# Kernel tuning notes

Measured on AMD Instinct MI355X. Metric: run time of the kernel, lower is better.

## Reference

```python
import jax, jax.numpy as jnp
import numpy as np

N = 4000      # number_of_sensors
D_IN = 128    # input feature dim
D_OUT = 128   # output feature dim
E_DIM = 16    # node embedding dim
B = 8         # batch size


def setup_inputs() -> dict:
    key = jax.random.key(0)
    k_x, k_e1, k_e2, k_w = jax.random.split(key, 4)
    x = jax.random.normal(k_x, (B, N, D_IN), dtype=jnp.float32)
    E1 = jax.random.normal(k_e1, (N, E_DIM), dtype=jnp.float32)
    E2 = jax.random.normal(k_e2, (N, E_DIM), dtype=jnp.float32)
    W = jax.random.normal(k_w, (D_IN, D_OUT), dtype=jnp.float32) * (1.0 / np.sqrt(D_IN))
    b = jnp.zeros((D_OUT,), dtype=jnp.float32)
    return {"x": x, "E1": E1, "E2": E2, "W": W, "b": b}


def reference(x, E1, E2, W, b):
    # Adaptive adjacency from node embeddings: A = softmax(relu(E1 @ E2^T), axis=-1)
    logits = jax.nn.relu(jnp.einsum('nd,md->nm', E1, E2))  # [N, N]
    adj = jax.nn.softmax(logits, axis=-1)                  # row-normalized adjacency
    # Graph aggregation then feature transform: relu(A @ X @ W + b)
    agg = jnp.einsum('nm,bmf->bnf', adj, x)                # [B, N, D_IN]
    out = jax.nn.relu(jnp.einsum('bnf,fo->bno', agg, W) + b)  # [B, N, D_OUT]
    return out
```

## Files before the change

kernel.cpp:

```cpp
#include <hip/hip_runtime.h>
#include <hip/hip_bf16.h>

#define NSEN 4000
#define NP   4096
#define DIN  128
#define DOUT 128
#define EDIM 16
#define BATCH 8

typedef __attribute__((ext_vector_type(8))) short bf16x8;
typedef __attribute__((ext_vector_type(4))) float f32x4;

__device__ __forceinline__ unsigned short f2bf(float f) {
  unsigned int u = __float_as_uint(f);
  unsigned int r = (u + 0x7FFFu + ((u >> 16) & 1u)) >> 16;
  return (unsigned short)r;
}
__device__ __forceinline__ float bf2f(unsigned short s) {
  unsigned int u = ((unsigned int)s) << 16;
  return __uint_as_float(u);
}

__device__ __forceinline__ void gl_lds16(const void* g, void* l) {
  __builtin_amdgcn_global_load_lds((const __attribute__((address_space(1))) void*)g,
                                   (__attribute__((address_space(3))) void*)l, 16, 0, 0);
}

__global__ __launch_bounds__(512) void k_prep(const float* __restrict__ E1,
                                              const float* __restrict__ E2,
                                              const float* __restrict__ W,
                                              const float* __restrict__ x,
                                              unsigned short* __restrict__ adjp,
                                              float* __restrict__ rinv,
                                              unsigned short* __restrict__ yt) {
  __shared__ float rsum[8][16];
  __shared__ unsigned short wlds[128 * 136];
  const int bx = blockIdx.x;
  const int tid = threadIdx.x;
  const int lane = tid & 63, wv = tid >> 6;
  const int lr = lane & 15, lq = lane >> 4;

  if (bx >= 250) {
    {
      const int fr = tid >> 5;
      const int o4 = tid & 31;
#pragma unroll
      for (int r8 = 0; r8 < 8; r8++) {
        const int f = fr + r8 * 16;
        float4 w4 = *(const float4*)&W[(size_t)f * DOUT + o4 * 4];
        wlds[(o4 * 4 + 0) * 136 + f] = f2bf(w4.x);
        wlds[(o4 * 4 + 1) * 136 + f] = f2bf(w4.y);
        wlds[(o4 * 4 + 2) * 136 + f] = f2bf(w4.z);
        wlds[(o4 * 4 + 3) * 136 + f] = f2bf(w4.w);
      }
    }
    __syncthreads();

    const int yi = bx - 250;
    const int b  = yi >> 4;
    const int m0 = (yi & 15) * 256;
    const int mh = wv >> 2;
    const int os = wv & 3;

    bf16x8 af[2][4];
#pragma unroll
    for (int ot = 0; ot < 2; ot++) {
      const int ob = os * 32 + ot * 16 + lr;
#pragma unroll
      for (int ks = 0; ks < 4; ks++)
        af[ot][ks] = *(const bf16x8*)&wlds[ob * 136 + ks * 32 + lq * 8];
    }

#pragma unroll
    for (int cc = 0; cc < 4; cc++) {
#pragma unroll
      for (int mtile = 0; mtile < 2; mtile++) {
        const int mb = m0 + cc * 64 + mh * 32 + mtile * 16;
        const int m = mb + lr;
        bf16x8 bx8[4];
        if (m < NSEN) {
          const float* xp = &x[((size_t)b * NSEN + m) * DIN + lq * 8];
#pragma unroll
          for (int ks = 0; ks < 4; ks++) {
            float4 v0 = *(const float4*)(xp + ks * 32);
            float4 v1 = *(const float4*)(xp + ks * 32 + 4);
            bx8[ks][0] = (short)f2bf(v0.x); bx8[ks][1] = (short)f2bf(v0.y);
            bx8[ks][2] = (short)f2bf(v0.z); bx8[ks][3] = (short)f2bf(v0.w);
            bx8[ks][4] = (short)f2bf(v1.x); bx8[ks][5] = (short)f2bf(v1.y);
            bx8[ks][6] = (short)f2bf(v1.z); bx8[ks][7] = (short)f2bf(v1.w);
          }
        } else {
#pragma unroll
          for (int ks = 0; ks < 4; ks++)
#pragma unroll
            for (int j = 0; j < 8; j++) bx8[ks][j] = 0;
        }
#pragma unroll
        for (int ot = 0; ot < 2; ot++) {
          f32x4 c = (f32x4){0.f, 0.f, 0.f, 0.f};
#pragma unroll
          for (int ks = 0; ks < 4; ks++)
            c = __builtin_amdgcn_mfma_f32_16x16x32_bf16(af[ot][ks], bx8[ks], c, 0, 0, 0);
#pragma unroll
          for (int i = 0; i < 4; i++)
            yt[(size_t)(b * 128 + os * 32 + ot * 16 + lq * 4 + i) * NP + mb + lr] = f2bf(c[i]);
        }
      }
    }
    return;
  }

  const int n0 = bx * 16;

  float a[8];
  {
    const float* e1p = &E1[(size_t)(n0 + lr) * EDIM + (lq & 1) * 8];
    *(float4*)&a[0] = *(const float4*)e1p;
    *(float4*)&a[4] = *(const float4*)(e1p + 4);
  }
  bf16x8 af1, af2;
#pragma unroll
  for (int j = 0; j < 8; j++) {
    unsigned short hs = f2bf(a[j]);
    af1[j] = (short)hs;
    float lo = a[j] - bf2f(hs);
    af2[j] = (lq < 2) ? (short)f2bf(lo) : (short)0;
  }

  float rs[4] = {0.f, 0.f, 0.f, 0.f};
  for (int t = wv; t < NSEN / 16; t += 8) {
    const int m = t * 16 + lr;
    float bv[8];
    const float* e2p = &E2[(size_t)m * EDIM + (lq & 1) * 8];
    *(float4*)&bv[0] = *(const float4*)e2p;
    *(float4*)&bv[4] = *(const float4*)(e2p + 4);
    bf16x8 bfrag;
#pragma unroll
    for (int j = 0; j < 8; j++) {
      unsigned short hs = f2bf(bv[j]);
      if (lq < 2) bfrag[j] = (short)hs;
      else        bfrag[j] = (short)f2bf(bv[j] - bf2f(hs));
    }
    f32x4 c = (f32x4){0.f, 0.f, 0.f, 0.f};
    c = __builtin_amdgcn_mfma_f32_16x16x32_bf16(af1, bfrag, c, 0, 0, 0);
    c = __builtin_amdgcn_mfma_f32_16x16x32_bf16(af2, bfrag, c, 0, 0, 0);
#pragma unroll
    for (int i = 0; i < 4; i++) {
      float p = __expf(fmaxf(c[i], 0.f));
      rs[i] += p;
      adjp[(size_t)(n0 + lq * 4 + i) * NP + t * 16 + lr] = f2bf(p);
    }
  }
  for (int i = tid; i < 16 * (NP - NSEN); i += 512) {
    int r = i / (NP - NSEN), c = i % (NP - NSEN);
    adjp[(size_t)(n0 + r) * NP + NSEN + c] = 0;
  }
#pragma unroll
  for (int i = 0; i < 4; i++) {
    rs[i] += __shfl_xor(rs[i], 1, 64);
    rs[i] += __shfl_xor(rs[i], 2, 64);
    rs[i] += __shfl_xor(rs[i], 4, 64);
    rs[i] += __shfl_xor(rs[i], 8, 64);
  }
  if (lr == 0) {
#pragma unroll
    for (int i = 0; i < 4; i++) rsum[wv][lq * 4 + i] = rs[i];
  }
  __syncthreads();
  if (tid < 16) {
    float s = 0.f;
#pragma unroll
    for (int w = 0; w < 8; w++) s += rsum[w][tid];
    rinv[n0 + tid] = 1.0f / s;
  }
}

__global__ __launch_bounds__(256, 2) void k_gemm1(const unsigned short* __restrict__ A,
                                                  const unsigned short* __restrict__ Bt,
                                                  unsigned short* __restrict__ part) {
  __shared__ __align__(16) unsigned short smem[32768];
  const int tid = threadIdx.x;
  const int lane = tid & 63, wv = tid >> 6;
  const int wr = wv >> 1, wc = wv & 1;
  const int lr = lane & 15, lq = lane >> 4;
  const int gx = blockIdx.x;
  const int m0 = (gx >> 1) * 128;
  const int kb0 = (gx & 1) * 2048;
  const int b  = blockIdx.y;
  const int c0 = b * 128;
  unsigned short* tA0 = smem;
  unsigned short* tB0 = smem + 16384;

  f32x4 acc[4][4];
#pragma unroll
  for (int p = 0; p < 4; p++)
#pragma unroll
    for (int q = 0; q < 4; q++) acc[p][q] = (f32x4){0.f, 0.f, 0.f, 0.f};

#define STAGE(bufi, kb)                                                              \
  {                                                                                  \
    _Pragma("unroll")                                                                \
    for (int s = 0; s < 4; s++) {                                                    \
      int idx = s * 256 + tid;                                                       \
      int row = idx >> 3;                                                            \
      int kc = ((idx & 7) ^ (row & 7)) << 3;                                         \
      gl_lds16(&A[(size_t)(m0 + row) * NP + (kb) + kc], &tA0[(bufi)*8192 + idx*8]);  \
      gl_lds16(&Bt[(size_t)(c0 + row) * NP + (kb) + kc], &tB0[(bufi)*8192 + idx*8]); \
    }                                                                                \
  }

  STAGE(0, kb0);

  for (int it = 0; it < 32; ++it) {
    const int cur = it & 1;
    if (it < 31) {
      STAGE(cur ^ 1, kb0 + (it + 1) * 64);
      asm volatile("s_waitcnt vmcnt(8)" ::: "memory");
    } else {
      asm volatile("s_waitcnt vmcnt(0)" ::: "memory");
    }
    __builtin_amdgcn_s_barrier();

    bf16x8 af0[4], bf0[4], af1[4], bf1[4];
    {
      const int koff0 = (lq * 8) ^ ((lr & 7) << 3);
#pragma unroll
      for (int p = 0; p < 4; p++)
        af0[p] = *(const bf16x8*)&tA0[cur * 8192 + (wr * 64 + p * 16 + lr) * 64 + koff0];
#pragma unroll
      for (int q = 0; q < 4; q++)
        bf0[q] = *(const bf16x8*)&tB0[cur * 8192 + (wc * 64 + q * 16 + lr) * 64 + koff0];
    }
    __builtin_amdgcn_sched_barrier(0);
    {
      const int koff1 = (32 + lq * 8) ^ ((lr & 7) << 3);
#pragma unroll
      for (int p = 0; p < 4; p++)
        af1[p] = *(const bf16x8*)&tA0[cur * 8192 + (wr * 64 + p * 16 + lr) * 64 + koff1];
#pragma unroll
      for (int q = 0; q < 4; q++)
        bf1[q] = *(const bf16x8*)&tB0[cur * 8192 + (wc * 64 + q * 16 + lr) * 64 + koff1];
    }
    asm volatile("s_waitcnt lgkmcnt(8)" ::: "memory");
    __builtin_amdgcn_sched_barrier(0);
    __builtin_amdgcn_s_setprio(1);
#pragma unroll
    for (int p = 0; p < 4; p++)
#pragma unroll
      for (int q = 0; q < 4; q++)
        acc[p][q] = __builtin_amdgcn_mfma_f32_16x16x32_bf16(af0[p], bf0[q], acc[p][q], 0, 0, 0);
    asm volatile("s_waitcnt lgkmcnt(0)" ::: "memory");
    __builtin_amdgcn_sched_barrier(0);
#pragma unroll
    for (int p = 0; p < 4; p++)
#pragma unroll
      for (int q = 0; q < 4; q++)
        acc[p][q] = __builtin_amdgcn_mfma_f32_16x16x32_bf16(af1[p], bf1[q], acc[p][q], 0, 0, 0);
    __builtin_amdgcn_s_setprio(0);
    __builtin_amdgcn_s_barrier();
  }
#undef STAGE

  const int kh = gx & 1;
  unsigned short* pdst = part + ((size_t)(kh * BATCH + b) * NP + m0) * DIN;
#pragma unroll
  for (int p = 0; p < 4; p++)
#pragma unroll
    for (int q = 0; q < 4; q++) {
      const int col = wc * 64 + q * 16 + lr;
#pragma unroll
      for (int i = 0; i < 4; i++) {
        const int row = wr * 64 + p * 16 + lq * 4 + i;
        pdst[row * DIN + col] = f2bf(acc[p][q][i]);
      }
    }
}

__global__ __launch_bounds__(256) void k_fin(const unsigned short* __restrict__ part,
                                             const float* __restrict__ rinv,
                                             const float* __restrict__ bias,
                                             float* __restrict__ out) {
  const int tid = threadIdx.x;
  const int nl = tid >> 4;
  const int ch = tid & 15;
  const int n  = blockIdx.x * 16 + nl;
  const int b  = blockIdx.y;
  const size_t base = ((size_t)b * NP + n) * DIN + ch * 8;
  const size_t khoff = (size_t)BATCH * NP * DIN;

  bf16x8 p0 = *(const bf16x8*)&part[base];
  bf16x8 p1 = *(const bf16x8*)&part[khoff + base];
  const float rv = rinv[n];
  float4 bb0 = *(const float4*)&bias[ch * 8];
  float4 bb1 = *(const float4*)&bias[ch * 8 + 4];
  float r[8];
#pragma unroll
  for (int j = 0; j < 8; j++) {
    float bbj = (j < 4) ? ((const float*)&bb0)[j] : ((const float*)&bb1)[j - 4];
    r[j] = fmaxf((bf2f((unsigned short)p0[j]) + bf2f((unsigned short)p1[j])) * rv + bbj, 0.f);
  }
  float* op = &out[((size_t)b * NSEN + n) * DOUT + ch * 8];
  *(float4*)op       = make_float4(r[0], r[1], r[2], r[3]);
  *(float4*)(op + 4) = make_float4(r[4], r[5], r[6], r[7]);
}

extern "C" void kernel_launch(void* const* d_in, const int* in_sizes, int n_in,
                              void* d_out, int out_size, void* d_ws, size_t ws_size,
                              hipStream_t stream) {
  const float* x    = (const float*)d_in[0];
  const float* E1   = (const float*)d_in[1];
  const float* E2   = (const float*)d_in[2];
  const float* W    = (const float*)d_in[3];
  const float* bias = (const float*)d_in[4];
  float* out = (float*)d_out;

  char* ws = (char*)d_ws;
  unsigned short* adjp = (unsigned short*)(ws);
  unsigned short* yt   = (unsigned short*)(ws + 33554432);
  float*          rinv = (float*)(ws + 33554432 + 8388608);
  unsigned short* part = (unsigned short*)(ws + 33554432 + 8388608 + 16384);

  k_prep<<<dim3(378), dim3(512), 0, stream>>>(E1, E2, W, x, adjp, rinv, yt);
  k_gemm1<<<dim3(64, BATCH), dim3(256), 0, stream>>>(adjp, yt, part);
  k_fin<<<dim3(250, BATCH), dim3(256), 0, stream>>>(part, rinv, bias, out);
}
```

Baseline: 77.46 us.

## Stage adjacency and Y writes through LDS, widen GEMM tiles, adaptive split-K

The prep kernel now stages the exp'd adjacency rows and the XW product in LDS before writing them back as coalesced 16-byte chunks, instead of scattering 2-byte stores. The Y-projection blocks are halved in size so more blocks share the work. The main GEMM becomes one 512-thread kernel with 256x256 tiles over a 4096x1024 output that covers all batches at once, and it picks 4-way or 2-way split-K depending on workspace size. The finalize kernel sums a variable number of K-slices. The costs are larger LDS and register use per block, and extra partial-sum traffic when 4-way split-K is chosen.

```diff
diff --git a/kernel.cpp b/kernel.cpp
--- a/kernel.cpp
+++ b/kernel.cpp
@@ -34,13 +34,15 @@
                                               float* __restrict__ rinv,
                                               unsigned short* __restrict__ yt) {
   __shared__ float rsum[8][16];
-  __shared__ unsigned short wlds[128 * 136];
+  __shared__ __align__(16) unsigned short pool[34816];
   const int bx = blockIdx.x;
   const int tid = threadIdx.x;
   const int lane = tid & 63, wv = tid >> 6;
   const int lr = lane & 15, lq = lane >> 4;
 
   if (bx >= 250) {
+    unsigned short* wlds = pool;
+    unsigned short* ylds = pool + 17408;
     {
       const int fr = tid >> 5;
       const int o4 = tid & 31;
@@ -57,8 +59,8 @@
     __syncthreads();
 
     const int yi = bx - 250;
-    const int b  = yi >> 4;
-    const int m0 = (yi & 15) * 256;
+    const int b  = yi >> 5;
+    const int m0 = (yi & 31) * 128;
     const int mh = wv >> 2;
     const int os = wv & 3;
 
@@ -72,44 +74,51 @@
     }
 
 #pragma unroll
-    for (int cc = 0; cc < 4; cc++) {
-#pragma unroll
-      for (int mtile = 0; mtile < 2; mtile++) {
-        const int mb = m0 + cc * 64 + mh * 32 + mtile * 16;
-        const int m = mb + lr;
-        bf16x8 bx8[4];
-        if (m < NSEN) {
-          const float* xp = &x[((size_t)b * NSEN + m) * DIN + lq * 8];
-#pragma unroll
-          for (int ks = 0; ks < 4; ks++) {
-            float4 v0 = *(const float4*)(xp + ks * 32);
-            float4 v1 = *(const float4*)(xp + ks * 32 + 4);
-            bx8[ks][0] = (short)f2bf(v0.x); bx8[ks][1] = (short)f2bf(v0.y);
-            bx8[ks][2] = (short)f2bf(v0.z); bx8[ks][3] = (short)f2bf(v0.w);
-            bx8[ks][4] = (short)f2bf(v1.x); bx8[ks][5] = (short)f2bf(v1.y);
-            bx8[ks][6] = (short)f2bf(v1.z); bx8[ks][7] = (short)f2bf(v1.w);
-          }
-        } else {
-#pragma unroll
-          for (int ks = 0; ks < 4; ks++)
-#pragma unroll
-            for (int j = 0; j < 8; j++) bx8[ks][j] = 0;
+    for (int mt = 0; mt < 4; mt++) {
+      const int mloc = mh * 64 + mt * 16;
+      const int m = m0 + mloc + lr;
+      bf16x8 bx8[4];
+      if (m < NSEN) {
+        const float* xp = &x[((size_t)b * NSEN + m) * DIN + lq * 8];
+#pragma unroll
+        for (int ks = 0; ks < 4; ks++) {
+          float4 v0 = *(const float4*)(xp + ks * 32);
+          float4 v1 = *(const float4*)(xp + ks * 32 + 4);
+          bx8[ks][0] = (short)f2bf(v0.x); bx8[ks][1] = (short)f2bf(v0.y);
+          bx8[ks][2] = (short)f2bf(v0.z); bx8[ks][3] = (short)f2bf(v0.w);
+          bx8[ks][4] = (short)f2bf(v1.x); bx8[ks][5] = (short)f2bf(v1.y);
+          bx8[ks][6] = (short)f2bf(v1.z); bx8[ks][7] = (short)f2bf(v1.w);
         }
-#pragma unroll
-        for (int ot = 0; ot < 2; ot++) {
-          f32x4 c = (f32x4){0.f, 0.f, 0.f, 0.f};
-#pragma unroll
-          for (int ks = 0; ks < 4; ks++)
-            c = __builtin_amdgcn_mfma_f32_16x16x32_bf16(af[ot][ks], bx8[ks], c, 0, 0, 0);
-#pragma unroll
-          for (int i = 0; i < 4; i++)
-            yt[(size_t)(b * 128 + os * 32 + ot * 16 + lq * 4 + i) * NP + mb + lr] = f2bf(c[i]);
-        }
-      }
+      } else {
+#pragma unroll
+        for (int ks = 0; ks < 4; ks++)
+#pragma unroll
+          for (int j = 0; j < 8; j++) bx8[ks][j] = 0;
+      }
+#pragma unroll
+      for (int ot = 0; ot < 2; ot++) {
+        f32x4 c = (f32x4){0.f, 0.f, 0.f, 0.f};
+#pragma unroll
+        for (int ks = 0; ks < 4; ks++)
+          c = __builtin_amdgcn_mfma_f32_16x16x32_bf16(af[ot][ks], bx8[ks], c, 0, 0, 0);
+#pragma unroll
+        for (int i = 0; i < 4; i++)
+          ylds[(os * 32 + ot * 16 + lq * 4 + i) * 136 + mloc + lr] = f2bf(c[i]);
+      }
+    }
+    __syncthreads();
+#pragma unroll
+    for (int s2 = 0; s2 < 4; s2++) {
+      int c = s2 * 512 + tid;
+      int row = c >> 4;
+      int mc = c & 15;
+      *(bf16x8*)&yt[(size_t)(b * 128 + row) * NP + m0 + mc * 8] =
+          *(const bf16x8*)&ylds[row * 136 + mc * 8];
     }
     return;
   }
 
+  unsigned short* bounce = pool;
   const int n0 = bx * 16;
 
   float a[8];
@@ -128,32 +137,46 @@
   }
 
   float rs[4] = {0.f, 0.f, 0.f, 0.f};
-  for (int t = wv; t < NSEN / 16; t += 8) {
-    const int m = t * 16 + lr;
-    float bv[8];
-    const float* e2p = &E2[(size_t)m * EDIM + (lq & 1) * 8];
-    *(float4*)&bv[0] = *(const float4*)e2p;
-    *(float4*)&bv[4] = *(const float4*)(e2p + 4);
-    bf16x8 bfrag;
-#pragma unroll
-    for (int j = 0; j < 8; j++) {
-      unsigned short hs = f2bf(bv[j]);
-      if (lq < 2) bfrag[j] = (short)hs;
-      else        bfrag[j] = (short)f2bf(bv[j] - bf2f(hs));
-    }
-    f32x4 c = (f32x4){0.f, 0.f, 0.f, 0.f};
-    c = __builtin_amdgcn_mfma_f32_16x16x32_bf16(af1, bfrag, c, 0, 0, 0);
-    c = __builtin_amdgcn_mfma_f32_16x16x32_bf16(af2, bfrag, c, 0, 0, 0);
-#pragma unroll
-    for (int i = 0; i < 4; i++) {
-      float p = __expf(fmaxf(c[i], 0.f));
-      rs[i] += p;
-      adjp[(size_t)(n0 + lq * 4 + i) * NP + t * 16 + lr] = f2bf(p);
-    }
-  }
-  for (int i = tid; i < 16 * (NP - NSEN); i += 512) {
-    int r = i / (NP - NSEN), c = i % (NP - NSEN);
-    adjp[(size_t)(n0 + r) * NP + NSEN + c] = 0;
+  for (int w0 = 0; w0 < 256; w0 += 64) {
+    if (w0 == 192) {
+      for (int z = tid; z < 16 * 96; z += 512) {
+        int zr = z / 96, zc = z % 96;
+        bounce[zr * 1040 + 58 * 16 + zc] = 0;
+      }
+    }
+    const int tend = (w0 + 64 < 250) ? (w0 + 64) : 250;
+    for (int t = w0 + wv; t < tend; t += 8) {
+      const int m = t * 16 + lr;
+      float bv[8];
+      const float* e2p = &E2[(size_t)m * EDIM + (lq & 1) * 8];
+      *(float4*)&bv[0] = *(const float4*)e2p;
+      *(float4*)&bv[4] = *(const float4*)(e2p + 4);
+      bf16x8 bfrag;
+#pragma unroll
+      for (int j = 0; j < 8; j++) {
+        unsigned short hs = f2bf(bv[j]);
+        if (lq < 2) bfrag[j] = (short)hs;
+        else        bfrag[j] = (short)f2bf(bv[j] - bf2f(hs));
+      }
+      f32x4 c = (f32x4){0.f, 0.f, 0.f, 0.f};
+      c = __builtin_amdgcn_mfma_f32_16x16x32_bf16(af1, bfrag, c, 0, 0, 0);
+      c = __builtin_amdgcn_mfma_f32_16x16x32_bf16(af2, bfrag, c, 0, 0, 0);
+#pragma unroll
+      for (int i = 0; i < 4; i++) {
+        float p = __expf(fmaxf(c[i], 0.f));
+        rs[i] += p;
+        bounce[(lq * 4 + i) * 1040 + (t - w0) * 16 + lr] = f2bf(p);
+      }
+    }
+    __syncthreads();
+#pragma unroll
+    for (int s2 = 0; s2 < 4; s2++) {
+      int cch = s2 * 512 + tid;
+      int row = cch >> 7, mc = cch & 127;
+      *(bf16x8*)&adjp[(size_t)(n0 + row) * NP + w0 * 16 + mc * 8] =
+          *(const bf16x8*)&bounce[row * 1040 + mc * 8];
+    }
+    __syncthreads();
   }
 #pragma unroll
   for (int i = 0; i < 4; i++) {
@@ -175,45 +198,45 @@
   }
 }
 
-__global__ __launch_bounds__(256, 2) void k_gemm1(const unsigned short* __restrict__ A,
-                                                  const unsigned short* __restrict__ Bt,
-                                                  unsigned short* __restrict__ part) {
-  __shared__ __align__(16) unsigned short smem[32768];
+__global__ __launch_bounds__(512, 2) void k_gemm(const unsigned short* __restrict__ A,
+                                                 const unsigned short* __restrict__ Bt,
+                                                 unsigned short* __restrict__ part,
+                                                 int nsteps) {
+  __shared__ __align__(16) unsigned short smem[65536];
+  unsigned short* tA0 = smem;
+  unsigned short* tB0 = smem + 32768;
   const int tid = threadIdx.x;
   const int lane = tid & 63, wv = tid >> 6;
-  const int wr = wv >> 1, wc = wv & 1;
+  const int wr = wv >> 2, wcn = wv & 3;
   const int lr = lane & 15, lq = lane >> 4;
-  const int gx = blockIdx.x;
-  const int m0 = (gx >> 1) * 128;
-  const int kb0 = (gx & 1) * 2048;
-  const int b  = blockIdx.y;
-  const int c0 = b * 128;
-  unsigned short* tA0 = smem;
-  unsigned short* tB0 = smem + 16384;
-
-  f32x4 acc[4][4];
-#pragma unroll
-  for (int p = 0; p < 4; p++)
+  const int kh = blockIdx.x >> 4;
+  const int m0 = (blockIdx.x & 15) * 256;
+  const int n0c = blockIdx.y * 256;
+  const int kb0 = kh * nsteps * 64;
+
+  f32x4 acc[8][4];
+#pragma unroll
+  for (int p = 0; p < 8; p++)
 #pragma unroll
     for (int q = 0; q < 4; q++) acc[p][q] = (f32x4){0.f, 0.f, 0.f, 0.f};
 
-#define STAGE(bufi, kb)                                                              \
-  {                                                                                  \
-    _Pragma("unroll")                                                                \
-    for (int s = 0; s < 4; s++) {                                                    \
-      int idx = s * 256 + tid;                                                       \
-      int row = idx >> 3;                                                            \
-      int kc = ((idx & 7) ^ (row & 7)) << 3;                                         \
-      gl_lds16(&A[(size_t)(m0 + row) * NP + (kb) + kc], &tA0[(bufi)*8192 + idx*8]);  \
-      gl_lds16(&Bt[(size_t)(c0 + row) * NP + (kb) + kc], &tB0[(bufi)*8192 + idx*8]); \
-    }                                                                                \
+#define STAGE(bufi, kb)                                                                 \
+  {                                                                                     \
+    _Pragma("unroll")                                                                   \
+    for (int s = 0; s < 4; s++) {                                                       \
+      int idx = s * 512 + tid;                                                          \
+      int row = idx >> 3;                                                               \
+      int kc = ((idx & 7) ^ (row & 7)) << 3;                                            \
+      gl_lds16(&A[(size_t)(m0 + row) * NP + (kb) + kc], &tA0[(bufi)*16384 + idx*8]);    \
+      gl_lds16(&Bt[(size_t)(n0c + row) * NP + (kb) + kc], &tB0[(bufi)*16384 + idx*8]);  \
+    }                                                                                   \
   }
 
   STAGE(0, kb0);
 
-  for (int it = 0; it < 32; ++it) {
+  for (int it = 0; it < nsteps; ++it) {
     const int cur = it & 1;
-    if (it < 31) {
+    if (it < nsteps - 1) {
       STAGE(cur ^ 1, kb0 + (it + 1) * 64);
       asm volatile("s_waitcnt vmcnt(8)" ::: "memory");
     } else {
@@ -221,57 +244,58 @@
     }
     __builtin_amdgcn_s_barrier();
 
-    bf16x8 af0[4], bf0[4], af1[4], bf1[4];
     {
-      const int koff0 = (lq * 8) ^ ((lr & 7) << 3);
-#pragma unroll
-      for (int p = 0; p < 4; p++)
-        af0[p] = *(const bf16x8*)&tA0[cur * 8192 + (wr * 64 + p * 16 + lr) * 64 + koff0];
+      const int koff = (lq * 8) ^ ((lr & 7) << 3);
+      bf16x8 af[8], bf[4];
+#pragma unroll
+      for (int p = 0; p < 8; p++)
+        af[p] = *(const bf16x8*)&tA0[cur * 16384 + (wr * 128 + p * 16 + lr) * 64 + koff];
 #pragma unroll
       for (int q = 0; q < 4; q++)
-        bf0[q] = *(const bf16x8*)&tB0[cur * 8192 + (wc * 64 + q * 16 + lr) * 64 + koff0];
-    }
-    __builtin_amdgcn_sched_barrier(0);
+        bf[q] = *(const bf16x8*)&tB0[cur * 16384 + (wcn * 64 + q * 16 + lr) * 64 + koff];
+      asm volatile("s_waitcnt lgkmcnt(0)" ::: "memory");
+      __builtin_amdgcn_sched_barrier(0);
+      __builtin_amdgcn_s_setprio(1);
+#pragma unroll
+      for (int p = 0; p < 8; p++)
+#pragma unroll
+        for (int q = 0; q < 4; q++)
+          acc[p][q] = __builtin_amdgcn_mfma_f32_16x16x32_bf16(af[p], bf[q], acc[p][q], 0, 0, 0);
+      __builtin_amdgcn_s_setprio(0);
+    }
     {
-      const int koff1 = (32 + lq * 8) ^ ((lr & 7) << 3);
-#pragma unroll
-      for (int p = 0; p < 4; p++)
-        af1[p] = *(const bf16x8*)&tA0[cur * 8192 + (wr * 64 + p * 16 + lr) * 64 + koff1];
+      const int koff = (32 + lq * 8) ^ ((lr & 7) << 3);
+      bf16x8 af[8], bf[4];
+#pragma unroll
+      for (int p = 0; p < 8; p++)
+        af[p] = *(const bf16x8*)&tA0[cur * 16384 + (wr * 128 + p * 16 + lr) * 64 + koff];
 #pragma unroll
       for (int q = 0; q < 4; q++)
-        bf1[q] = *(const bf16x8*)&tB0[cur * 8192 + (wc * 64 + q * 16 + lr) * 64 + koff1];
-    }
-    asm volatile("s_waitcnt lgkmcnt(8)" ::: "memory");
-    __builtin_amdgcn_sched_barrier(0);
-    __builtin_amdgcn_s_setprio(1);
-#pragma unroll
-    for (int p = 0; p < 4; p++)
-#pragma unroll
-      for (int q = 0; q < 4; q++)
-        acc[p][q] = __builtin_amdgcn_mfma_f32_16x16x32_bf16(af0[p], bf0[q], acc[p][q], 0, 0, 0);
-    asm volatile("s_waitcnt lgkmcnt(0)" ::: "memory");
-    __builtin_amdgcn_sched_barrier(0);
-#pragma unroll
-    for (int p = 0; p < 4; p++)
-#pragma unroll
-      for (int q = 0; q < 4; q++)
-        acc[p][q] = __builtin_amdgcn_mfma_f32_16x16x32_bf16(af1[p], bf1[q], acc[p][q], 0, 0, 0);
-    __builtin_amdgcn_s_setprio(0);
+        bf[q] = *(const bf16x8*)&tB0[cur * 16384 + (wcn * 64 + q * 16 + lr) * 64 + koff];
+      asm volatile("s_waitcnt lgkmcnt(0)" ::: "memory");
+      __builtin_amdgcn_sched_barrier(0);
+      __builtin_amdgcn_s_setprio(1);
+#pragma unroll
+      for (int p = 0; p < 8; p++)
+#pragma unroll
+        for (int q = 0; q < 4; q++)
+          acc[p][q] = __builtin_amdgcn_mfma_f32_16x16x32_bf16(af[p], bf[q], acc[p][q], 0, 0, 0);
+      __builtin_amdgcn_s_setprio(0);
+    }
     __builtin_amdgcn_s_barrier();
   }
 #undef STAGE
 
-  const int kh = gx & 1;
-  unsigned short* pdst = part + ((size_t)(kh * BATCH + b) * NP + m0) * DIN;
-#pragma unroll
-  for (int p = 0; p < 4; p++)
+  unsigned short* pdst = part + ((size_t)kh << 22);
+#pragma unroll
+  for (int p = 0; p < 8; p++)
 #pragma unroll
     for (int q = 0; q < 4; q++) {
-      const int col = wc * 64 + q * 16 + lr;
+      const int col = n0c + wcn * 64 + q * 16 + lr;
 #pragma unroll
       for (int i = 0; i < 4; i++) {
-        const int row = wr * 64 + p * 16 + lq * 4 + i;
-        pdst[row * DIN + col] = f2bf(acc[p][q][i]);
+        const int row = m0 + wr * 128 + p * 16 + lq * 4 + i;
+        pdst[(size_t)row * 1024 + col] = f2bf(acc[p][q][i]);
       }
     }
 }
@@ -279,25 +303,28 @@
 __global__ __launch_bounds__(256) void k_fin(const unsigned short* __restrict__ part,
                                              const float* __restrict__ rinv,
                                              const float* __restrict__ bias,
-                                             float* __restrict__ out) {
+                                             float* __restrict__ out, int ksl) {
   const int tid = threadIdx.x;
   const int nl = tid >> 4;
   const int ch = tid & 15;
   const int n  = blockIdx.x * 16 + nl;
   const int b  = blockIdx.y;
-  const size_t base = ((size_t)b * NP + n) * DIN + ch * 8;
-  const size_t khoff = (size_t)BATCH * NP * DIN;
-
-  bf16x8 p0 = *(const bf16x8*)&part[base];
-  bf16x8 p1 = *(const bf16x8*)&part[khoff + base];
+  const int j  = b * 128 + ch * 8;
+
+  float s[8] = {0.f, 0.f, 0.f, 0.f, 0.f, 0.f, 0.f, 0.f};
+  for (int kh = 0; kh < ksl; kh++) {
+    bf16x8 pv = *(const bf16x8*)&part[((size_t)kh << 22) + (size_t)n * 1024 + j];
+#pragma unroll
+    for (int jj = 0; jj < 8; jj++) s[jj] += bf2f((unsigned short)pv[jj]);
+  }
   const float rv = rinv[n];
   float4 bb0 = *(const float4*)&bias[ch * 8];
   float4 bb1 = *(const float4*)&bias[ch * 8 + 4];
   float r[8];
 #pragma unroll
-  for (int j = 0; j < 8; j++) {
-    float bbj = (j < 4) ? ((const float*)&bb0)[j] : ((const float*)&bb1)[j - 4];
-    r[j] = fmaxf((bf2f((unsigned short)p0[j]) + bf2f((unsigned short)p1[j])) * rv + bbj, 0.f);
+  for (int jj = 0; jj < 8; jj++) {
+    float bbj = (jj < 4) ? ((const float*)&bb0)[jj] : ((const float*)&bb1)[jj - 4];
+    r[jj] = fmaxf(s[jj] * rv + bbj, 0.f);
   }
   float* op = &out[((size_t)b * NSEN + n) * DOUT + ch * 8];
   *(float4*)op       = make_float4(r[0], r[1], r[2], r[3]);
@@ -320,7 +347,11 @@
   float*          rinv = (float*)(ws + 33554432 + 8388608);
   unsigned short* part = (unsigned short*)(ws + 33554432 + 8388608 + 16384);
 
-  k_prep<<<dim3(378), dim3(512), 0, stream>>>(E1, E2, W, x, adjp, rinv, yt);
-  k_gemm1<<<dim3(64, BATCH), dim3(256), 0, stream>>>(adjp, yt, part);
-  k_fin<<<dim3(250, BATCH), dim3(256), 0, stream>>>(part, rinv, bias, out);
-}
+  const size_t need4 = 33554432ull + 8388608 + 16384 + 4ull * 8388608;
+  const int KS = (ws_size >= need4) ? 4 : 2;
+  const int nsteps = 64 / KS;
+
+  k_prep<<<dim3(506), dim3(512), 0, stream>>>(E1, E2, W, x, adjp, rinv, yt);
+  k_gemm<<<dim3(KS * 16, 4), dim3(512), 0, stream>>>(adjp, yt, part, nsteps);
+  k_fin<<<dim3(250, BATCH), dim3(256), 0, stream>>>(part, rinv, bias, out, KS);
+}
```

New measurement: 81.75 us. 5.5% more time.
